# Kernel tuning notes

Measured on AMD Instinct MI355X. Metric: run time of the kernel, lower is better.

## Reference

```python
import jax, jax.numpy as jnp
import numpy as np

B, C_IN, C_OUT, N, K = 1, 64, 64, 50000, 20


def setup_inputs() -> dict:
    key = jax.random.key(0)
    k1, k2, k3, k4, k5 = jax.random.split(key, 5)
    x = jax.random.normal(k1, (B, C_IN, N, 1), dtype=jnp.float32)
    edge_index = jax.random.randint(k2, (2, B, N, K), 0, N, dtype=jnp.int64)
    dis = jax.random.uniform(k3, (B, N, K), dtype=jnp.float32)
    W = jax.random.normal(k4, (C_OUT, 2 * C_IN), dtype=jnp.float32) * (2.0 / (2 * C_IN)) ** 0.5
    b = jnp.zeros((C_OUT,), dtype=jnp.float32)
    att_w = jax.random.normal(k5, (K,), dtype=jnp.float32) * (2.0 / K) ** 0.5
    att_b = jnp.zeros((1,), dtype=jnp.float32)
    return {"x": x, "edge_index": edge_index, "dis": dis, "W": W, "b": b,
            "att_w": att_w, "att_b": att_b}


def reference(x, edge_index, dis, W, b, att_w, att_b):
    # x: [B, C, N, 1]; edge_index: [2, B, N, K]; dis: [B, N, K]
    x2 = x[..., 0]  # [B, C, N]
    gather = jax.vmap(lambda xb, ib: xb[:, ib])  # per-batch: [C,N] idx[N,K] -> [C,N,K]
    x_i = gather(x2, edge_index[1])  # [B, C, N, K]
    x_j = gather(x2, edge_index[0])  # [B, C, N, K]
    feat = jnp.concatenate([x_i, x_j - x_i], axis=1)  # [B, 2C, N, K]
    # 1x1 conv == channel contraction
    feat = jax.nn.relu(jnp.einsum('oc,bcnk->bonk', W, feat) + b[None, :, None, None])
    # attention over the k channel of dis -> per-node scaler
    scaler = jnp.tanh(jnp.einsum('k,bnk->bn', att_w, dis) + att_b) + 1.0  # [B, N]
    suppression = 2.0 * jax.nn.sigmoid(-dis * scaler[:, :, None])  # [B, N, K]
    feat = feat * suppression[:, None, :, :]  # [B, C_out, N, K]
    return jnp.max(feat, axis=-1, keepdims=True)  # [B, C_out, N, 1]
```

## Files before the change

### kernel.cpp

```cpp
#include <hip/hip_runtime.h>

#define NN 50000
#define KK 20

__device__ __align__(256) ushort g_poolA[NN * 64];
__device__ __align__(256) ushort g_poolB[NN * 64];
__device__ __align__(256) float  g_sup[NN * KK];

static __device__ __forceinline__ ushort f2bf(float f) {
    unsigned int u = __float_as_uint(f);
    unsigned int r = (u + 0x7FFFu + ((u >> 16) & 1u)) >> 16;
    return (ushort)r;
}
static __device__ __forceinline__ float bfl(unsigned int u) {
    return __uint_as_float(u << 16);
}
static __device__ __forceinline__ float bfh(unsigned int u) {
    return __uint_as_float(u & 0xffff0000u);
}

__global__ __launch_bounds__(256) void prep_kernel(
    const float* __restrict__ x,
    const float* __restrict__ W,
    const float* __restrict__ b,
    const float* __restrict__ dis,
    const float* __restrict__ att_w,
    const float* __restrict__ att_b)
{
    __shared__ float At[64][66];
    __shared__ float Bt[64][66];
    __shared__ float xt[64][132];
    __shared__ float disL[128 * KK];
    __shared__ float scalerL[128];

    const int t  = threadIdx.x;
    const int n0 = blockIdx.x * 128;

    for (int i = t; i < 64 * 64; i += 256) {
        int c = i >> 6, ci = i & 63;
        float w1 = W[c * 128 + ci];
        float w2 = W[c * 128 + 64 + ci];
        At[ci][c] = w1 - w2;
        Bt[ci][c] = w2;
    }
    {
        const int q  = t & 31;
        const int cb = t >> 5;
        const float4* x4 = (const float4*)x;
        const int nq = (n0 >> 2) + q;
        #pragma unroll
        for (int i = 0; i < 8; i++) {
            const int ci = cb * 8 + i;
            float4 v = (nq < 12500) ? x4[ci * 12500 + nq]
                                    : float4{0.f, 0.f, 0.f, 0.f};
            *(float4*)&xt[ci][q * 4] = v;
        }
    }
    for (int i = t; i < 128 * KK; i += 256) {
        const int gi = n0 * KK + i;
        disL[i] = (gi < NN * KK) ? dis[gi] : 0.f;
    }
    __syncthreads();

    if (t < 128) {
        float z = att_b[0];
        #pragma unroll
        for (int k = 0; k < KK; k++) z += att_w[k] * disL[t * KK + k];
        scalerL[t] = 2.f / (1.f + __expf(-2.f * z));
    }
    __syncthreads();

    for (int i = t; i < 128 * KK; i += 256) {
        const int gi = n0 * KK + i;
        if (gi < NN * KK)
            g_sup[gi] = 2.f / (1.f + __expf(disL[i] * scalerL[i / KK]));
    }

    const int c2 = t & 31;
    const int g  = t >> 5;

    float aA0[16], aA1[16], aB0[16], aB1[16];
    #pragma unroll
    for (int j = 0; j < 16; j++) { aA0[j]=0.f; aA1[j]=0.f; aB0[j]=0.f; aB1[j]=0.f; }

    for (int ci = 0; ci < 64; ci++) {
        const float2 a  = *(const float2*)&At[ci][c2 * 2];
        const float2 w2 = *(const float2*)&Bt[ci][c2 * 2];
        const float4* xr = (const float4*)&xt[ci][g * 16];
        #pragma unroll
        for (int q = 0; q < 4; q++) {
            float4 xv = xr[q];
            aA0[q*4+0] += a.x*xv.x;  aA1[q*4+0] += a.y*xv.x;
            aB0[q*4+0] += w2.x*xv.x; aB1[q*4+0] += w2.y*xv.x;
            aA0[q*4+1] += a.x*xv.y;  aA1[q*4+1] += a.y*xv.y;
            aB0[q*4+1] += w2.x*xv.y; aB1[q*4+1] += w2.y*xv.y;
            aA0[q*4+2] += a.x*xv.z;  aA1[q*4+2] += a.y*xv.z;
            aB0[q*4+2] += w2.x*xv.z; aB1[q*4+2] += w2.y*xv.z;
            aA0[q*4+3] += a.x*xv.w;  aA1[q*4+3] += a.y*xv.w;
            aB0[q*4+3] += w2.x*xv.w; aB1[q*4+3] += w2.y*xv.w;
        }
    }

    const float b0 = b[c2 * 2], b1 = b[c2 * 2 + 1];
    unsigned int* yA32 = (unsigned int*)g_poolA;
    unsigned int* yB32 = (unsigned int*)g_poolB;
    #pragma unroll
    for (int j = 0; j < 16; j++) {
        const int n = n0 + g * 16 + j;
        if (n < NN) {
            yA32[n * 32 + c2] = (unsigned int)f2bf(aA0[j] + b0)
                              | ((unsigned int)f2bf(aA1[j] + b1) << 16);
            yB32[n * 32 + c2] = (unsigned int)f2bf(aB0[j])
                              | ((unsigned int)f2bf(aB1[j]) << 16);
        }
    }
}

__global__ __launch_bounds__(256) void edge_kernel(
    const int* __restrict__ ej,
    const int* __restrict__ ei,
    float* __restrict__ out)
{
    __shared__ float tile[16][68];

    const int t    = threadIdx.x;
    const int lane = t & 63;
    const int w    = t >> 6;
    const int g    = lane >> 4;
    const int l    = lane & 15;
    const int n0   = blockIdx.x * 16;
    const int nb   = n0 + w * 4;

    const char* pA = (const char*)g_poolA;
    const char* pB = (const char*)g_poolB;

    int offI[4], offJ[4]; float sup4[4];
    #pragma unroll
    for (int s = 0; s < 4; s++) {
        const int n = nb + s;
        int ii = 0, jj = 0; float sp = 0.f;
        if (lane < KK) {
            ii = __builtin_nontemporal_load(&ei[n * KK + lane]);
            jj = __builtin_nontemporal_load(&ej[n * KK + lane]);
            sp = __builtin_nontemporal_load(&g_sup[n * KK + lane]);
        }
        offI[s] = ii << 7;
        offJ[s] = jj << 7;
        sup4[s] = sp;
    }

    #pragma unroll
    for (int s = 0; s < 4; s++) {
        float4 m = {0.f, 0.f, 0.f, 0.f};
        #pragma unroll
        for (int kb = 0; kb < 5; kb++) {
            const int   src = kb * 4 + g;
            const int   oi  = __shfl(offI[s], src);
            const int   oj  = __shfl(offJ[s], src);
            const float sp  = __shfl(sup4[s], src);
            const uint2 a   = *(const uint2*)(pA + oi + l * 8);
            const uint2 bb  = *(const uint2*)(pB + oj + l * 8);
            float v;
            v = fmaxf(bfl(a.x) + bfl(bb.x), 0.f) * sp;  m.x = fmaxf(m.x, v);
            v = fmaxf(bfh(a.x) + bfh(bb.x), 0.f) * sp;  m.y = fmaxf(m.y, v);
            v = fmaxf(bfl(a.y) + bfl(bb.y), 0.f) * sp;  m.z = fmaxf(m.z, v);
            v = fmaxf(bfh(a.y) + bfh(bb.y), 0.f) * sp;  m.w = fmaxf(m.w, v);
        }
        #pragma unroll
        for (int mask = 16; mask <= 32; mask <<= 1) {
            m.x = fmaxf(m.x, __shfl_xor(m.x, mask));
            m.y = fmaxf(m.y, __shfl_xor(m.y, mask));
            m.z = fmaxf(m.z, __shfl_xor(m.z, mask));
            m.w = fmaxf(m.w, __shfl_xor(m.w, mask));
        }
        if (g == 0) *(float4*)&tile[w * 4 + s][l * 4] = m;
    }
    __syncthreads();

    #pragma unroll
    for (int it = 0; it < 4; it++) {
        const int c  = it * 16 + (t >> 4);
        const int nl = t & 15;
        __builtin_nontemporal_store(tile[nl][c],
                                    &out[(size_t)c * NN + n0 + nl]);
    }
}

extern "C" void kernel_launch(void* const* d_in, const int* in_sizes, int n_in,
                              void* d_out, int out_size, void* d_ws, size_t ws_size,
                              hipStream_t stream) {
    const float* x     = (const float*)d_in[0];
    const int*   e     = (const int*)d_in[1];
    const float* dis   = (const float*)d_in[2];
    const float* W     = (const float*)d_in[3];
    const float* b     = (const float*)d_in[4];
    const float* att_w = (const float*)d_in[5];
    const float* att_b = (const float*)d_in[6];
    float* out = (float*)d_out;

    (void)d_ws; (void)ws_size;

    prep_kernel<<<(NN + 127) / 128, 256, 0, stream>>>(x, W, b, dis, att_w, att_b);
    edge_kernel<<<NN / 16, 256, 0, stream>>>(e, e + NN * KK, out);
}
```

Baseline: 133.5 us.

## Split gather pools into four channel groups for per-XCD L2 locality

Stores the bf16 A/B projection pools as four 16-channel groups and launches four times as many edge blocks, each handling one channel group. Because group is chosen by blockIdx&3, round-robin block placement over XCDs should keep each XCD on a single group, so its gather working set can stay in that XCD's L2. The costs are that edge indices and suppression values are reloaded four times, and each node's 20 edges are spread over 32 lane slots, leaving some lanes idle.

```diff
diff --git a/kernel.cpp b/kernel.cpp
--- a/kernel.cpp
+++ b/kernel.cpp
@@ -3,8 +3,7 @@
 #define NN 50000
 #define KK 20
 
-__device__ __align__(256) ushort g_poolA[NN * 64];
-__device__ __align__(256) ushort g_poolB[NN * 64];
+__device__ __align__(256) ushort g_pool[4][2][NN * 16];
 __device__ __align__(256) float  g_sup[NN * KK];
 
 static __device__ __forceinline__ ushort f2bf(float f) {
@@ -102,16 +101,19 @@
     }
 
     const float b0 = b[c2 * 2], b1 = b[c2 * 2 + 1];
-    unsigned int* yA32 = (unsigned int*)g_poolA;
-    unsigned int* yB32 = (unsigned int*)g_poolB;
+    const int gq = c2 >> 3;
+    const int pp = c2 & 7;
+    unsigned int* poolU = (unsigned int*)g_pool;
+    const size_t pa = (size_t)(gq * 2 + 0) * NN * 8;
+    const size_t pb = (size_t)(gq * 2 + 1) * NN * 8;
     #pragma unroll
     for (int j = 0; j < 16; j++) {
         const int n = n0 + g * 16 + j;
         if (n < NN) {
-            yA32[n * 32 + c2] = (unsigned int)f2bf(aA0[j] + b0)
-                              | ((unsigned int)f2bf(aA1[j] + b1) << 16);
-            yB32[n * 32 + c2] = (unsigned int)f2bf(aB0[j])
-                              | ((unsigned int)f2bf(aB1[j]) << 16);
+            poolU[pa + (size_t)n * 8 + pp] = (unsigned int)f2bf(aA0[j] + b0)
+                                           | ((unsigned int)f2bf(aA1[j] + b1) << 16);
+            poolU[pb + (size_t)n * 8 + pp] = (unsigned int)f2bf(aB0[j])
+                                           | ((unsigned int)f2bf(aB1[j]) << 16);
         }
     }
 }
@@ -121,18 +123,20 @@
     const int* __restrict__ ei,
     float* __restrict__ out)
 {
-    __shared__ float tile[16][68];
+    __shared__ float tile[16][20];
 
     const int t    = threadIdx.x;
     const int lane = t & 63;
     const int w    = t >> 6;
-    const int g    = lane >> 4;
-    const int l    = lane & 15;
-    const int n0   = blockIdx.x * 16;
+    const int g2   = lane >> 2;
+    const int q    = lane & 3;
+    const int bx   = blockIdx.x;
+    const int grp  = bx & 3;
+    const int n0   = (bx >> 2) * 16;
     const int nb   = n0 + w * 4;
 
-    const char* pA = (const char*)g_poolA;
-    const char* pB = (const char*)g_poolB;
+    const char* pA = (const char*)&g_pool[grp][0][0];
+    const char* pB = (const char*)&g_pool[grp][1][0];
 
     int offI[4], offJ[4]; float sup4[4];
     #pragma unroll
@@ -144,8 +148,8 @@
             jj = __builtin_nontemporal_load(&ej[n * KK + lane]);
             sp = __builtin_nontemporal_load(&g_sup[n * KK + lane]);
         }
-        offI[s] = ii << 7;
-        offJ[s] = jj << 7;
+        offI[s] = ii << 5;
+        offJ[s] = jj << 5;
         sup4[s] = sp;
     }
 
@@ -153,13 +157,13 @@
     for (int s = 0; s < 4; s++) {
         float4 m = {0.f, 0.f, 0.f, 0.f};
         #pragma unroll
-        for (int kb = 0; kb < 5; kb++) {
-            const int   src = kb * 4 + g;
+        for (int r = 0; r < 2; r++) {
+            const int   src = r * 16 + g2;
             const int   oi  = __shfl(offI[s], src);
             const int   oj  = __shfl(offJ[s], src);
             const float sp  = __shfl(sup4[s], src);
-            const uint2 a   = *(const uint2*)(pA + oi + l * 8);
-            const uint2 bb  = *(const uint2*)(pB + oj + l * 8);
+            const uint2 a   = *(const uint2*)(pA + oi + q * 8);
+            const uint2 bb  = *(const uint2*)(pB + oj + q * 8);
             float v;
             v = fmaxf(bfl(a.x) + bfl(bb.x), 0.f) * sp;  m.x = fmaxf(m.x, v);
             v = fmaxf(bfh(a.x) + bfh(bb.x), 0.f) * sp;  m.y = fmaxf(m.y, v);
@@ -167,22 +171,21 @@
             v = fmaxf(bfh(a.y) + bfh(bb.y), 0.f) * sp;  m.w = fmaxf(m.w, v);
         }
         #pragma unroll
-        for (int mask = 16; mask <= 32; mask <<= 1) {
+        for (int mask = 4; mask <= 32; mask <<= 1) {
             m.x = fmaxf(m.x, __shfl_xor(m.x, mask));
             m.y = fmaxf(m.y, __shfl_xor(m.y, mask));
             m.z = fmaxf(m.z, __shfl_xor(m.z, mask));
             m.w = fmaxf(m.w, __shfl_xor(m.w, mask));
         }
-        if (g == 0) *(float4*)&tile[w * 4 + s][l * 4] = m;
+        if (g2 == 0) *(float4*)&tile[w * 4 + s][q * 4] = m;
     }
     __syncthreads();
 
-    #pragma unroll
-    for (int it = 0; it < 4; it++) {
-        const int c  = it * 16 + (t >> 4);
+    {
+        const int c  = t >> 4;
         const int nl = t & 15;
         __builtin_nontemporal_store(tile[nl][c],
-                                    &out[(size_t)c * NN + n0 + nl]);
+                                    &out[(size_t)(grp * 16 + c) * NN + n0 + nl]);
     }
 }
 
@@ -201,5 +204,5 @@
     (void)d_ws; (void)ws_size;
 
     prep_kernel<<<(NN + 127) / 128, 256, 0, stream>>>(x, W, b, dis, att_w, att_b);
-    edge_kernel<<<NN / 16, 256, 0, stream>>>(e, e + NN * KK, out);
-}
+    edge_kernel<<<4 * (NN / 16), 256, 0, stream>>>(e, e + NN * KK, out);
+}
```

Result: slower. 170.2 us (+27.5%).
